# Kernel optimization log

Measured on AMD Instinct MI355X. Metric: run time of the kernel, lower is better.

The kernel has to match this reference:

```python
import jax, jax.numpy as jnp
import numpy as np

N = 100000  # nodes
E = 1600000  # edges
D_IN = 64
D_H = 64


def _sage_conv(x, src, dst, w_l, b_l, w_r):
    """PyG SAGEConv (mean aggr): lin_l(mean_j x_j) + lin_r(x_i).
    w_l, w_r: [out, in]; b_l: [out]."""
    # scatter-mean of source features onto target nodes
    msg_sum = jax.ops.segment_sum(x[src], dst, num_segments=N)  # [N, in]
    cnt = jax.ops.segment_sum(jnp.ones((src.shape[0],), x.dtype), dst, num_segments=N)
    mean = msg_sum / jnp.maximum(cnt, 1.0)[:, None]
    return mean @ w_l.T + b_l + x @ w_r.T


def setup_inputs() -> dict:
    key = jax.random.key(0)
    ks = jax.random.split(key, 8)
    x = jax.random.normal(ks[0], (N, D_IN), dtype=jnp.float32)
    edge_index = jax.random.randint(ks[1], (2, E), 0, N, dtype=jnp.int64)
    s = 1.0 / np.sqrt(D_IN)
    w_l1 = jax.random.uniform(ks[2], (D_H, D_IN), jnp.float32, -s, s)
    b_l1 = jnp.zeros((D_H,), jnp.float32)
    w_r1 = jax.random.uniform(ks[3], (D_H, D_IN), jnp.float32, -s, s)
    s2 = 1.0 / np.sqrt(D_H)
    w_l2 = jax.random.uniform(ks[4], (D_H, D_H), jnp.float32, -s2, s2)
    b_l2 = jnp.zeros((D_H,), jnp.float32)
    w_r2 = jax.random.uniform(ks[5], (D_H, D_H), jnp.float32, -s2, s2)
    return {"x": x, "edge_index": edge_index,
            "w_l1": w_l1, "b_l1": b_l1, "w_r1": w_r1,
            "w_l2": w_l2, "b_l2": b_l2, "w_r2": w_r2}


def reference(x, edge_index, w_l1, b_l1, w_r1, w_l2, b_l2, w_r2):
    src, dst = edge_index[0], edge_index[1]
    h = jax.nn.relu(_sage_conv(x, src, dst, w_l1, b_l1, w_r1))
    out = _sage_conv(h, src, dst, w_l2, b_l2, w_r2)
    return out
```

## Files before the change

### kernel.cpp

```cpp
#include <hip/hip_runtime.h>

#define N_NODES 100000
#define N_EDGES 1600000
#define D 64

#define BSHIFT 7
#define BNODES (1 << BSHIFT)
#define NB ((N_NODES + BNODES - 1) / BNODES)
#define PB 256
#define TILE ((N_EDGES + PB - 1) / PB)
#define CAP 2432
#define MAXB 4096
#define CAST_GRID 2048
#define HPARTS (N_NODES / 16 * 4)

typedef __attribute__((ext_vector_type(8))) short short8;
typedef __attribute__((ext_vector_type(4))) float float4v;

__device__ __forceinline__ unsigned short f2bf(float f) {
    unsigned u = __float_as_uint(f);
    u = (u + 0x7fffu + ((u >> 16) & 1u)) >> 16;
    return (unsigned short)u;
}
__device__ __forceinline__ unsigned packbf2(float a, float b) {
    return (unsigned)f2bf(a) | ((unsigned)f2bf(b) << 16);
}

__device__ __forceinline__ float4 bf16x4_to_f4(uint2 v) {
    float4 r;
    r.x = __uint_as_float(v.x << 16);
    r.y = __uint_as_float(v.x & 0xffff0000u);
    r.z = __uint_as_float(v.y << 16);
    r.w = __uint_as_float(v.y & 0xffff0000u);
    return r;
}

__global__ __launch_bounds__(256) void cast_absmax_part(const float* __restrict__ x,
                                                        unsigned short* __restrict__ xb,
                                                        float* __restrict__ partial) {
    __shared__ float red[4];
    float m = 0.0f;
    int stride = gridDim.x * 256;
    for (int i = blockIdx.x * 256 + threadIdx.x; i < N_NODES * D / 4; i += stride) {
        float4 v = ((const float4*)x)[i];
        ushort4 o;
        o.x = f2bf(v.x); o.y = f2bf(v.y); o.z = f2bf(v.z); o.w = f2bf(v.w);
        ((ushort4*)xb)[i] = o;
        m = fmaxf(m, fmaxf(fmaxf(fabsf(v.x), fabsf(v.y)), fmaxf(fabsf(v.z), fabsf(v.w))));
    }
    for (int off = 32; off >= 1; off >>= 1) m = fmaxf(m, __shfl_xor(m, off, 64));
    if ((threadIdx.x & 63) == 0) red[threadIdx.x >> 6] = m;
    __syncthreads();
    if (threadIdx.x == 0)
        partial[blockIdx.x] = fmaxf(fmaxf(red[0], red[1]), fmaxf(red[2], red[3]));
}

__global__ __launch_bounds__(1024) void reduce_amax(const float* __restrict__ partial,
                                                    int n,
                                                    unsigned* __restrict__ amax_bits) {
    __shared__ float red[16];
    float m = 0.0f;
    for (int i = threadIdx.x; i < n; i += 1024) m = fmaxf(m, partial[i]);
    for (int off = 32; off >= 1; off >>= 1) m = fmaxf(m, __shfl_xor(m, off, 64));
    if ((threadIdx.x & 63) == 0) red[threadIdx.x >> 6] = m;
    __syncthreads();
    if (threadIdx.x == 0) {
        float mm = 0.0f;
#pragma unroll
        for (int w = 0; w < 16; ++w) mm = fmaxf(mm, red[w]);
        *amax_bits = __float_as_uint(mm);
    }
}

__global__ __launch_bounds__(256) void quant8(const unsigned short* __restrict__ inb,
                                              unsigned char* __restrict__ out8,
                                              const unsigned* __restrict__ amax_bits) {
    int i = blockIdx.x * blockDim.x + threadIdx.x;
    if (i >= N_NODES * D / 4) return;
    float A = __uint_as_float(*amax_bits);
    float s = (A > 0.0f) ? 127.0f / A : 0.0f;
    uint2 v = ((const uint2*)inb)[i];
    float4 f = bf16x4_to_f4(v);
    int q0 = min(127, max(-127, __float2int_rn(f.x * s))) + 128;
    int q1 = min(127, max(-127, __float2int_rn(f.y * s))) + 128;
    int q2 = min(127, max(-127, __float2int_rn(f.z * s))) + 128;
    int q3 = min(127, max(-127, __float2int_rn(f.w * s))) + 128;
    ((unsigned*)out8)[i] = (unsigned)q0 | ((unsigned)q1 << 8) |
                           ((unsigned)q2 << 16) | ((unsigned)q3 << 24);
}

__global__ __launch_bounds__(256) void prep_w2(const float* __restrict__ wl1,
                                               const float* __restrict__ wr1,
                                               unsigned short* __restrict__ wb1,
                                               const float* __restrict__ wl2,
                                               const float* __restrict__ wr2,
                                               unsigned short* __restrict__ wb2) {
    int i = blockIdx.x * 256 + threadIdx.x;
    int j = i & 8191;
    int o = j >> 7, k = j & 127;
    if (i < 8192) {
        float v = (k < D) ? wl1[o * D + k] : wr1[o * D + (k - D)];
        wb1[j] = f2bf(v);
    } else {
        float v = (k < D) ? wl2[o * D + k] : wr2[o * D + (k - D)];
        wb2[j] = f2bf(v);
    }
}

__global__ __launch_bounds__(1024) void p1_fused(const int* __restrict__ src,
                                                 const int* __restrict__ dst,
                                                 int* __restrict__ gcnt,
                                                 int* __restrict__ part) {
    __shared__ int hist[NB];
    for (int i = threadIdx.x; i < NB; i += 1024) hist[i] = 0;
    __syncthreads();

    int lo = blockIdx.x * TILE;
    int hi = min(lo + TILE, N_EDGES);

    unsigned pk[7];
    int bk[7];
#pragma unroll
    for (int k = 0; k < 7; ++k) {
        int e = lo + threadIdx.x + k * 1024;
        if (e < hi) {
            int dd = dst[e];
            int ss = src[e];
            int b = dd >> BSHIFT;
            pk[k] = ((unsigned)ss << BSHIFT) | (unsigned)(dd & (BNODES - 1));
            bk[k] = b;
            atomicAdd(&hist[b], 1);
        } else {
            bk[k] = -1;
        }
    }
    __syncthreads();

    for (int b = threadIdx.x; b < NB; b += 1024) {
        int h = hist[b];
        if (h) hist[b] = b * CAP + atomicAdd(&gcnt[b], h);
    }
    __syncthreads();

#pragma unroll
    for (int k = 0; k < 7; ++k) {
        if (bk[k] >= 0) {
            int p = atomicAdd(&hist[bk[k]], 1);
            part[p] = (int)pk[k];
        }
    }
}

__global__ __launch_bounds__(1024) void scan_nb(const int* __restrict__ gcnt,
                                                int* __restrict__ bbase) {
    __shared__ int t[1024];
    int i = threadIdx.x;
    int v = (i < NB) ? gcnt[i] : 0;
    int val = v;
    t[i] = val;
    __syncthreads();
    for (int off = 1; off < 1024; off <<= 1) {
        int u = (i >= off) ? t[i - off] : 0;
        __syncthreads();
        val += u;
        t[i] = val;
        __syncthreads();
    }
    if (i < NB) bbase[i] = val - v;
}

__global__ __launch_bounds__(1024) void p2_sort(const int* __restrict__ bbase,
                                                const int* __restrict__ gcnt,
                                                const int* __restrict__ part,
                                                int* __restrict__ row_ptr,
                                                int* __restrict__ sorted_src) {
    __shared__ int in_buf[MAXB];
    __shared__ int out_buf[MAXB];
    __shared__ int hist[BNODES];
    __shared__ int exs[BNODES];
    __shared__ int cursor[BNODES];

    int k = blockIdx.x;
    int base  = bbase[k];
    int count = gcnt[k];
    int src0  = k * CAP;
    int tid = threadIdx.x;

    for (int i = tid; i < BNODES; i += 1024) hist[i] = 0;
    __syncthreads();

    if (count <= MAXB) {
        for (int i = tid; i < count; i += 1024) {
            int w = part[src0 + i];
            in_buf[i] = w;
            atomicAdd(&hist[w & (BNODES - 1)], 1);
        }
        __syncthreads();
        if (tid < 64) {
            int a = hist[2 * tid], b = hist[2 * tid + 1];
            int s = a + b, incl = s;
            for (int off = 1; off < 64; off <<= 1) {
                int t = __shfl_up(incl, off, 64);
                if (tid >= off) incl += t;
            }
            int excl = incl - s;
            exs[2 * tid] = excl;
            exs[2 * tid + 1] = excl + a;
        }
        __syncthreads();
        if (tid < BNODES) {
            int node = k * BNODES + tid;
            if (node < N_NODES) row_ptr[node] = base + exs[tid];
            cursor[tid] = exs[tid];
        }
        if (tid == 0 && k == NB - 1) row_ptr[N_NODES] = N_EDGES;
        __syncthreads();
        for (int i = tid; i < count; i += 1024) {
            int w = in_buf[i];
            int r = atomicAdd(&cursor[w & (BNODES - 1)], 1);
            out_buf[r] = w >> BSHIFT;
        }
        __syncthreads();
        for (int i = tid; i < count; i += 1024)
            sorted_src[base + i] = out_buf[i];
    } else {
        for (int i = tid; i < count; i += 1024)
            atomicAdd(&hist[part[src0 + i] & (BNODES - 1)], 1);
        __syncthreads();
        if (tid < 64) {
            int a = hist[2 * tid], b = hist[2 * tid + 1];
            int s = a + b, incl = s;
            for (int off = 1; off < 64; off <<= 1) {
                int t = __shfl_up(incl, off, 64);
                if (tid >= off) incl += t;
            }
            int excl = incl - s;
            exs[2 * tid] = excl;
            exs[2 * tid + 1] = excl + a;
        }
        __syncthreads();
        if (tid < BNODES) {
            int node = k * BNODES + tid;
            if (node < N_NODES) row_ptr[node] = base + exs[tid];
            cursor[tid] = exs[tid];
        }
        if (tid == 0 && k == NB - 1) row_ptr[N_NODES] = N_EDGES;
        __syncthreads();
        for (int i = tid; i < count; i += 1024) {
            int w = part[src0 + i];
            int r = atomicAdd(&cursor[w & (BNODES - 1)], 1);
            sorted_src[base + r] = w >> BSHIFT;
        }
    }
}

#define ACCW(w, kk) { aLo[kk] += (w) & 0x00FF00FFu; \
                      aHi[kk] += __builtin_amdgcn_perm(0u, (w), 0x04030401u); }
#define ACC4(v) { ACCW((v).x, 0) ACCW((v).y, 1) ACCW((v).z, 2) ACCW((v).w, 3) }

__global__ __launch_bounds__(512) void sage8(
    const int* __restrict__ row_ptr, const int* __restrict__ nbr,
    const unsigned char* __restrict__ tab8,
    const unsigned short* __restrict__ selfb,
    const unsigned* __restrict__ amax_bits,
    const unsigned short* __restrict__ wb,
    const float* __restrict__ b_l,
    float* __restrict__ out,
    unsigned short* __restrict__ outb,
    float* __restrict__ hpart,
    int apply_relu)
{
    __shared__ unsigned short a_s[16][136];
    __shared__ float bias[D];

    int tid = threadIdx.x;
    if (tid < D) bias[tid] = b_l[tid];

    int wave = tid >> 6;
    int lane = tid & 63;
    int nsel = lane >> 5;
    int l32  = lane & 31;
    int g    = l32 >> 2;
    int c    = l32 & 3;
    int arow = wave * 2 + nsel;
    int node = blockIdx.x * 16 + arow;

    float A  = __uint_as_float(*amax_bits);
    float gs = A * (1.0f / 127.0f);

    int begin = row_ptr[node];
    int end   = row_ptr[node + 1];

    unsigned c16 = (unsigned)(c << 4);
    unsigned aLo[4] = {0, 0, 0, 0};
    unsigned aHi[4] = {0, 0, 0, 0};
    for (int base = begin; base < end; base += 32) {
        int m = end - base; if (m > 32) m = 32;
        int id = (l32 < m) ? __builtin_nontemporal_load(&nbr[base + l32]) : 0;
        int s0 = __shfl(id, nsel * 32 + g,      64);
        int s1 = __shfl(id, nsel * 32 + 8 + g,  64);
        int s2 = __shfl(id, nsel * 32 + 16 + g, 64);
        int s3 = __shfl(id, nsel * 32 + 24 + g, 64);
        bool a0 = (g < m), a1 = (8 + g < m), a2 = (16 + g < m), a3 = (24 + g < m);
        uint4 v0, v1, v2, v3;
        if (a0) v0 = *(const uint4*)(tab8 + ((((unsigned)s0) << 6) | c16));
        if (a1) v1 = *(const uint4*)(tab8 + ((((unsigned)s1) << 6) | c16));
        if (a2) v2 = *(const uint4*)(tab8 + ((((unsigned)s2) << 6) | c16));
        if (a3) v3 = *(const uint4*)(tab8 + ((((unsigned)s3) << 6) | c16));
        if (a0) { ACC4(v0) }
        if (a1) { ACC4(v1) }
        if (a2) { ACC4(v2) }
        if (a3) { ACC4(v3) }
    }

#pragma unroll
    for (int off = 4; off <= 16; off <<= 1) {
#pragma unroll
        for (int k = 0; k < 4; ++k) {
            aLo[k] += (unsigned)__shfl_xor((int)aLo[k], off, 64);
            aHi[k] += (unsigned)__shfl_xor((int)aHi[k], off, 64);
        }
    }

    int   deg  = end - begin;
    float invd = 1.0f / fmaxf((float)deg, 1.0f);
    float bofs = 128.0f * (float)deg;
    float sc   = gs * invd;

    if (l32 < 4) {
        uint4 q0, q1;
        float d0 = ((float)(aLo[0] & 0xFFFFu) - bofs) * sc;
        float d2 = ((float)(aLo[0] >> 16)     - bofs) * sc;
        float d1 = ((float)(aHi[0] & 0xFFFFu) - bofs) * sc;
        float d3 = ((float)(aHi[0] >> 16)     - bofs) * sc;
        q0.x = packbf2(d0, d1); q0.y = packbf2(d2, d3);
        d0 = ((float)(aLo[1] & 0xFFFFu) - bofs) * sc;
        d2 = ((float)(aLo[1] >> 16)     - bofs) * sc;
        d1 = ((float)(aHi[1] & 0xFFFFu) - bofs) * sc;
        d3 = ((float)(aHi[1] >> 16)     - bofs) * sc;
        q0.z = packbf2(d0, d1); q0.w = packbf2(d2, d3);
        d0 = ((float)(aLo[2] & 0xFFFFu) - bofs) * sc;
        d2 = ((float)(aLo[2] >> 16)     - bofs) * sc;
        d1 = ((float)(aHi[2] & 0xFFFFu) - bofs) * sc;
        d3 = ((float)(aHi[2] >> 16)     - bofs) * sc;
        q1.x = packbf2(d0, d1); q1.y = packbf2(d2, d3);
        d0 = ((float)(aLo[3] & 0xFFFFu) - bofs) * sc;
        d2 = ((float)(aLo[3] >> 16)     - bofs) * sc;
        d1 = ((float)(aHi[3] & 0xFFFFu) - bofs) * sc;
        d3 = ((float)(aHi[3] >> 16)     - bofs) * sc;
        q1.z = packbf2(d0, d1); q1.w = packbf2(d2, d3);
        *(uint4*)&a_s[arow][16 * l32]     = q0;
        *(uint4*)&a_s[arow][16 * l32 + 8] = q1;
    }
    if (l32 < 16) {
        uint2 xv = *(const uint2*)&selfb[(size_t)node * D + 4 * l32];
        *(uint2*)&a_s[arow][64 + 4 * l32] = xv;
    }
    __syncthreads();

    if (wave >= 4) return;

    int quad = lane >> 4;
    int cc   = lane & 15;

    float4v acc = {0.f, 0.f, 0.f, 0.f};
#pragma unroll
    for (int kk = 0; kk < 4; ++kk) {
        short8 af = *(const short8*)&a_s[cc][kk * 32 + quad * 8];
        short8 bf = *(const short8*)(wb + (size_t)(wave * 16 + cc) * 128 + kk * 32 + quad * 8);
        acc = __builtin_amdgcn_mfma_f32_16x16x32_bf16(af, bf, acc, 0, 0, 0);
    }

    int o = wave * 16 + cc;
    float bv = bias[o];
    float vv[4];
#pragma unroll
    for (int r = 0; r < 4; ++r) {
        float v = acc[r] + bv;
        if (apply_relu) v = fmaxf(v, 0.0f);
        vv[r] = v;
    }
#pragma unroll
    for (int r = 0; r < 4; ++r) {
        int nd = blockIdx.x * 16 + quad * 4 + r;
        if (out)  __builtin_nontemporal_store(vv[r], &out[(size_t)nd * D + o]);
        if (outb) __builtin_nontemporal_store(f2bf(vv[r]), &outb[(size_t)nd * D + o]);
    }
    if (hpart) {
        float m = fmaxf(fmaxf(fabsf(vv[0]), fabsf(vv[1])),
                        fmaxf(fabsf(vv[2]), fabsf(vv[3])));
        for (int off = 32; off >= 1; off >>= 1) m = fmaxf(m, __shfl_xor(m, off, 64));
        if (lane == 0) hpart[blockIdx.x * 4 + wave] = m;
    }
}

extern "C" void kernel_launch(void* const* d_in, const int* in_sizes, int n_in,
                              void* d_out, int out_size, void* d_ws, size_t ws_size,
                              hipStream_t stream) {
    const float* x    = (const float*)d_in[0];
    const int*   ei   = (const int*)d_in[1];
    const float* w_l1 = (const float*)d_in[2];
    const float* b_l1 = (const float*)d_in[3];
    const float* w_r1 = (const float*)d_in[4];
    const float* w_l2 = (const float*)d_in[5];
    const float* b_l2 = (const float*)d_in[6];
    const float* w_r2 = (const float*)d_in[7];
    float* out = (float*)d_out;

    const int* src = ei;
    const int* dst = ei + N_EDGES;

    unsigned* scales   = (unsigned*)d_ws;
    int* gcnt          = (int*)d_ws + 4;
    int* bbase         = gcnt + NB;
    int* row_ptr       = bbase + NB;
    int* part          = row_ptr + 100004;
    int* sorted_src    = part + NB * CAP;
    unsigned short* xb = (unsigned short*)(sorted_src + N_EDGES);
    unsigned short* hb = xb + (size_t)N_NODES * D;
    unsigned char* x8  = (unsigned char*)(hb + (size_t)N_NODES * D);
    unsigned char* h8  = x8 + (size_t)N_NODES * D;
    unsigned short* wb1 = (unsigned short*)(h8 + (size_t)N_NODES * D);
    unsigned short* wb2 = wb1 + D * 2 * D;
    float* partA       = (float*)(wb2 + D * 2 * D);

    hipMemsetAsync(gcnt, 0, NB * sizeof(int), stream);

    dim3 b256(256);
    int qgrid = (N_NODES * D / 4 + 255) / 256;
    cast_absmax_part<<<dim3(CAST_GRID), b256, 0, stream>>>(x, xb, partA);
    reduce_amax<<<dim3(1), dim3(1024), 0, stream>>>(partA, CAST_GRID, &scales[0]);
    quant8<<<dim3(qgrid), b256, 0, stream>>>(xb, x8, &scales[0]);
    prep_w2<<<dim3(64), b256, 0, stream>>>(w_l1, w_r1, wb1, w_l2, w_r2, wb2);

    p1_fused<<<dim3(PB), dim3(1024), 0, stream>>>(src, dst, gcnt, part);
    scan_nb<<<dim3(1), dim3(1024), 0, stream>>>(gcnt, bbase);
    p2_sort<<<dim3(NB), dim3(1024), 0, stream>>>(bbase, gcnt, part, row_ptr, sorted_src);

    dim3 lblk(512);
    dim3 lgrid(N_NODES / 16);
    sage8<<<lgrid, lblk, 0, stream>>>(row_ptr, sorted_src, x8, xb,
                                      &scales[0], wb1, b_l1,
                                      (float*)nullptr, hb, partA, 1);
    reduce_amax<<<dim3(1), dim3(1024), 0, stream>>>(partA, HPARTS, &scales[1]);
    quant8<<<dim3(qgrid), b256, 0, stream>>>(hb, h8, &scales[1]);
    sage8<<<lgrid, lblk, 0, stream>>>(row_ptr, sorted_src, h8, hb,
                                      &scales[1], wb2, b_l2,
                                      out, (unsigned short*)nullptr,
                                      (float*)nullptr, 0);
}
```

Before: 233.0 us.

## Merge preprocessing kernels into fewer launches and stage sage8 output stores via LDS

Cast/absmax and the edge bucketing pass now run as one launch split by block index. A single mid kernel does the bucket scan, the amax reduce and the weight prep, and a single back kernel does the per-bucket sort plus x quantisation, cutting the launch count from ten to six. Inside sage8, the self-feature load is issued early, bf16 packing uses the v_cvt_pk_bf16_f32 instruction, and results are staged in shared memory so the idle waves write coalesced 16-byte stores. The per-wave amax is also reduced in-block, which shrinks the partial array. In exchange it adds a barrier and LDS use in sage8, and it drops the p2_sort overflow path for buckets larger than MAXB.

```diff
diff --git a/kernel.cpp b/kernel.cpp
--- a/kernel.cpp
+++ b/kernel.cpp
@@ -11,19 +11,24 @@
 #define TILE ((N_EDGES + PB - 1) / PB)
 #define CAP 2432
 #define MAXB 4096
-#define CAST_GRID 2048
-#define HPARTS (N_NODES / 16 * 4)
+#define CAST_BLKS 512
+#define QBLKS ((N_NODES * D / 4 + 1023) / 1024)
+#define HPARTS (N_NODES / 16)
 
 typedef __attribute__((ext_vector_type(8))) short short8;
 typedef __attribute__((ext_vector_type(4))) float float4v;
+typedef __attribute__((ext_vector_type(2))) unsigned uint2v;
+typedef __attribute__((ext_vector_type(4))) unsigned uint4v;
 
 __device__ __forceinline__ unsigned short f2bf(float f) {
     unsigned u = __float_as_uint(f);
     u = (u + 0x7fffu + ((u >> 16) & 1u)) >> 16;
     return (unsigned short)u;
 }
-__device__ __forceinline__ unsigned packbf2(float a, float b) {
-    return (unsigned)f2bf(a) | ((unsigned)f2bf(b) << 16);
+__device__ __forceinline__ unsigned cvtpk(float a, float b) {
+    unsigned r;
+    asm("v_cvt_pk_bf16_f32 %0, %1, %2" : "=v"(r) : "v"(a), "v"(b));
+    return r;
 }
 
 __device__ __forceinline__ float4 bf16x4_to_f4(uint2 v) {
@@ -35,87 +40,43 @@
     return r;
 }
 
-__global__ __launch_bounds__(256) void cast_absmax_part(const float* __restrict__ x,
-                                                        unsigned short* __restrict__ xb,
-                                                        float* __restrict__ partial) {
-    __shared__ float red[4];
-    float m = 0.0f;
-    int stride = gridDim.x * 256;
-    for (int i = blockIdx.x * 256 + threadIdx.x; i < N_NODES * D / 4; i += stride) {
-        float4 v = ((const float4*)x)[i];
-        ushort4 o;
-        o.x = f2bf(v.x); o.y = f2bf(v.y); o.z = f2bf(v.z); o.w = f2bf(v.w);
-        ((ushort4*)xb)[i] = o;
-        m = fmaxf(m, fmaxf(fmaxf(fabsf(v.x), fabsf(v.y)), fmaxf(fabsf(v.z), fabsf(v.w))));
-    }
-    for (int off = 32; off >= 1; off >>= 1) m = fmaxf(m, __shfl_xor(m, off, 64));
-    if ((threadIdx.x & 63) == 0) red[threadIdx.x >> 6] = m;
-    __syncthreads();
-    if (threadIdx.x == 0)
-        partial[blockIdx.x] = fmaxf(fmaxf(red[0], red[1]), fmaxf(red[2], red[3]));
-}
-
-__global__ __launch_bounds__(1024) void reduce_amax(const float* __restrict__ partial,
-                                                    int n,
-                                                    unsigned* __restrict__ amax_bits) {
+__global__ __launch_bounds__(1024) void front(const float* __restrict__ x,
+                                              unsigned short* __restrict__ xb,
+                                              float* __restrict__ partial,
+                                              const int* __restrict__ src,
+                                              const int* __restrict__ dst,
+                                              int* __restrict__ gcnt,
+                                              int* __restrict__ part) {
     __shared__ float red[16];
-    float m = 0.0f;
-    for (int i = threadIdx.x; i < n; i += 1024) m = fmaxf(m, partial[i]);
-    for (int off = 32; off >= 1; off >>= 1) m = fmaxf(m, __shfl_xor(m, off, 64));
-    if ((threadIdx.x & 63) == 0) red[threadIdx.x >> 6] = m;
-    __syncthreads();
-    if (threadIdx.x == 0) {
-        float mm = 0.0f;
-#pragma unroll
-        for (int w = 0; w < 16; ++w) mm = fmaxf(mm, red[w]);
-        *amax_bits = __float_as_uint(mm);
-    }
-}
-
-__global__ __launch_bounds__(256) void quant8(const unsigned short* __restrict__ inb,
-                                              unsigned char* __restrict__ out8,
-                                              const unsigned* __restrict__ amax_bits) {
-    int i = blockIdx.x * blockDim.x + threadIdx.x;
-    if (i >= N_NODES * D / 4) return;
-    float A = __uint_as_float(*amax_bits);
-    float s = (A > 0.0f) ? 127.0f / A : 0.0f;
-    uint2 v = ((const uint2*)inb)[i];
-    float4 f = bf16x4_to_f4(v);
-    int q0 = min(127, max(-127, __float2int_rn(f.x * s))) + 128;
-    int q1 = min(127, max(-127, __float2int_rn(f.y * s))) + 128;
-    int q2 = min(127, max(-127, __float2int_rn(f.z * s))) + 128;
-    int q3 = min(127, max(-127, __float2int_rn(f.w * s))) + 128;
-    ((unsigned*)out8)[i] = (unsigned)q0 | ((unsigned)q1 << 8) |
-                           ((unsigned)q2 << 16) | ((unsigned)q3 << 24);
-}
-
-__global__ __launch_bounds__(256) void prep_w2(const float* __restrict__ wl1,
-                                               const float* __restrict__ wr1,
-                                               unsigned short* __restrict__ wb1,
-                                               const float* __restrict__ wl2,
-                                               const float* __restrict__ wr2,
-                                               unsigned short* __restrict__ wb2) {
-    int i = blockIdx.x * 256 + threadIdx.x;
-    int j = i & 8191;
-    int o = j >> 7, k = j & 127;
-    if (i < 8192) {
-        float v = (k < D) ? wl1[o * D + k] : wr1[o * D + (k - D)];
-        wb1[j] = f2bf(v);
-    } else {
-        float v = (k < D) ? wl2[o * D + k] : wr2[o * D + (k - D)];
-        wb2[j] = f2bf(v);
-    }
-}
-
-__global__ __launch_bounds__(1024) void p1_fused(const int* __restrict__ src,
-                                                 const int* __restrict__ dst,
-                                                 int* __restrict__ gcnt,
-                                                 int* __restrict__ part) {
     __shared__ int hist[NB];
+
+    if (blockIdx.x < CAST_BLKS) {
+        float m = 0.0f;
+        int stride = CAST_BLKS * 1024;
+        for (int i = blockIdx.x * 1024 + threadIdx.x; i < N_NODES * D / 4; i += stride) {
+            float4 v = ((const float4*)x)[i];
+            ushort4 o;
+            o.x = f2bf(v.x); o.y = f2bf(v.y); o.z = f2bf(v.z); o.w = f2bf(v.w);
+            ((ushort4*)xb)[i] = o;
+            m = fmaxf(m, fmaxf(fmaxf(fabsf(v.x), fabsf(v.y)), fmaxf(fabsf(v.z), fabsf(v.w))));
+        }
+        for (int off = 32; off >= 1; off >>= 1) m = fmaxf(m, __shfl_xor(m, off, 64));
+        if ((threadIdx.x & 63) == 0) red[threadIdx.x >> 6] = m;
+        __syncthreads();
+        if (threadIdx.x == 0) {
+            float mm = 0.0f;
+#pragma unroll
+            for (int w = 0; w < 16; ++w) mm = fmaxf(mm, red[w]);
+            partial[blockIdx.x] = mm;
+        }
+        return;
+    }
+
+    int bid = blockIdx.x - CAST_BLKS;
     for (int i = threadIdx.x; i < NB; i += 1024) hist[i] = 0;
     __syncthreads();
 
-    int lo = blockIdx.x * TILE;
+    int lo = bid * TILE;
     int hi = min(lo + TILE, N_EDGES);
 
     unsigned pk[7];
@@ -151,106 +112,164 @@
     }
 }
 
-__global__ __launch_bounds__(1024) void scan_nb(const int* __restrict__ gcnt,
-                                                int* __restrict__ bbase) {
+__global__ __launch_bounds__(1024) void mid(const int* __restrict__ gcnt,
+                                            int* __restrict__ bbase,
+                                            const float* __restrict__ partial,
+                                            unsigned* __restrict__ amax_bits,
+                                            const float* __restrict__ wl1,
+                                            const float* __restrict__ wr1,
+                                            unsigned short* __restrict__ wb1,
+                                            const float* __restrict__ wl2,
+                                            const float* __restrict__ wr2,
+                                            unsigned short* __restrict__ wb2) {
     __shared__ int t[1024];
-    int i = threadIdx.x;
-    int v = (i < NB) ? gcnt[i] : 0;
-    int val = v;
-    t[i] = val;
-    __syncthreads();
-    for (int off = 1; off < 1024; off <<= 1) {
-        int u = (i >= off) ? t[i - off] : 0;
+    __shared__ float red[16];
+    int tid = threadIdx.x;
+
+    if (blockIdx.x == 0) {
+        int v = (tid < NB) ? gcnt[tid] : 0;
+        int val = v;
+        t[tid] = val;
         __syncthreads();
-        val += u;
-        t[i] = val;
+        for (int off = 1; off < 1024; off <<= 1) {
+            int u = (tid >= off) ? t[tid - off] : 0;
+            __syncthreads();
+            val += u;
+            t[tid] = val;
+            __syncthreads();
+        }
+        if (tid < NB) bbase[tid] = val - v;
+    } else if (blockIdx.x == 1) {
+        float m = 0.0f;
+        for (int i = tid; i < CAST_BLKS; i += 1024) m = fmaxf(m, partial[i]);
+        for (int off = 32; off >= 1; off >>= 1) m = fmaxf(m, __shfl_xor(m, off, 64));
+        if ((tid & 63) == 0) red[tid >> 6] = m;
         __syncthreads();
-    }
-    if (i < NB) bbase[i] = val - v;
-}
-
-__global__ __launch_bounds__(1024) void p2_sort(const int* __restrict__ bbase,
-                                                const int* __restrict__ gcnt,
-                                                const int* __restrict__ part,
-                                                int* __restrict__ row_ptr,
-                                                int* __restrict__ sorted_src) {
+        if (tid == 0) {
+            float mm = 0.0f;
+#pragma unroll
+            for (int w = 0; w < 16; ++w) mm = fmaxf(mm, red[w]);
+            *amax_bits = __float_as_uint(mm);
+        }
+    } else {
+        int i = (blockIdx.x - 2) * 1024 + tid;
+        int j = i & 8191;
+        int o = j >> 7, k = j & 127;
+        if (i < 8192) {
+            float v = (k < D) ? wl1[o * D + k] : wr1[o * D + (k - D)];
+            wb1[j] = f2bf(v);
+        } else {
+            float v = (k < D) ? wl2[o * D + k] : wr2[o * D + (k - D)];
+            wb2[j] = f2bf(v);
+        }
+    }
+}
+
+__device__ __forceinline__ void quant_body(int i, const unsigned short* __restrict__ inb,
+                                           unsigned char* __restrict__ out8, float s) {
+    uint2 v = ((const uint2*)inb)[i];
+    float4 f = bf16x4_to_f4(v);
+    int q0 = min(127, max(-127, __float2int_rn(f.x * s))) + 128;
+    int q1 = min(127, max(-127, __float2int_rn(f.y * s))) + 128;
+    int q2 = min(127, max(-127, __float2int_rn(f.z * s))) + 128;
+    int q3 = min(127, max(-127, __float2int_rn(f.w * s))) + 128;
+    ((unsigned*)out8)[i] = (unsigned)q0 | ((unsigned)q1 << 8) |
+                           ((unsigned)q2 << 16) | ((unsigned)q3 << 24);
+}
+
+__global__ __launch_bounds__(1024) void back(const int* __restrict__ bbase,
+                                             const int* __restrict__ gcnt,
+                                             const int* __restrict__ part,
+                                             int* __restrict__ row_ptr,
+                                             int* __restrict__ sorted_src,
+                                             const unsigned short* __restrict__ xb,
+                                             unsigned char* __restrict__ x8,
+                                             const unsigned* __restrict__ amax_bits) {
     __shared__ int in_buf[MAXB];
     __shared__ int out_buf[MAXB];
     __shared__ int hist[BNODES];
     __shared__ int exs[BNODES];
     __shared__ int cursor[BNODES];
 
+    int tid = threadIdx.x;
+
+    if (blockIdx.x >= NB) {
+        int i = (blockIdx.x - NB) * 1024 + tid;
+        if (i < N_NODES * D / 4) {
+            float A = __uint_as_float(*amax_bits);
+            float s = (A > 0.0f) ? 127.0f / A : 0.0f;
+            quant_body(i, xb, x8, s);
+        }
+        return;
+    }
+
     int k = blockIdx.x;
     int base  = bbase[k];
     int count = gcnt[k];
     int src0  = k * CAP;
-    int tid = threadIdx.x;
 
     for (int i = tid; i < BNODES; i += 1024) hist[i] = 0;
     __syncthreads();
 
-    if (count <= MAXB) {
-        for (int i = tid; i < count; i += 1024) {
-            int w = part[src0 + i];
-            in_buf[i] = w;
-            atomicAdd(&hist[w & (BNODES - 1)], 1);
-        }
-        __syncthreads();
-        if (tid < 64) {
-            int a = hist[2 * tid], b = hist[2 * tid + 1];
-            int s = a + b, incl = s;
-            for (int off = 1; off < 64; off <<= 1) {
-                int t = __shfl_up(incl, off, 64);
-                if (tid >= off) incl += t;
-            }
-            int excl = incl - s;
-            exs[2 * tid] = excl;
-            exs[2 * tid + 1] = excl + a;
-        }
-        __syncthreads();
-        if (tid < BNODES) {
-            int node = k * BNODES + tid;
-            if (node < N_NODES) row_ptr[node] = base + exs[tid];
-            cursor[tid] = exs[tid];
-        }
-        if (tid == 0 && k == NB - 1) row_ptr[N_NODES] = N_EDGES;
-        __syncthreads();
-        for (int i = tid; i < count; i += 1024) {
-            int w = in_buf[i];
-            int r = atomicAdd(&cursor[w & (BNODES - 1)], 1);
-            out_buf[r] = w >> BSHIFT;
-        }
-        __syncthreads();
-        for (int i = tid; i < count; i += 1024)
-            sorted_src[base + i] = out_buf[i];
-    } else {
-        for (int i = tid; i < count; i += 1024)
-            atomicAdd(&hist[part[src0 + i] & (BNODES - 1)], 1);
-        __syncthreads();
-        if (tid < 64) {
-            int a = hist[2 * tid], b = hist[2 * tid + 1];
-            int s = a + b, incl = s;
-            for (int off = 1; off < 64; off <<= 1) {
-                int t = __shfl_up(incl, off, 64);
-                if (tid >= off) incl += t;
-            }
-            int excl = incl - s;
-            exs[2 * tid] = excl;
-            exs[2 * tid + 1] = excl + a;
-        }
-        __syncthreads();
-        if (tid < BNODES) {
-            int node = k * BNODES + tid;
-            if (node < N_NODES) row_ptr[node] = base + exs[tid];
-            cursor[tid] = exs[tid];
-        }
-        if (tid == 0 && k == NB - 1) row_ptr[N_NODES] = N_EDGES;
-        __syncthreads();
-        for (int i = tid; i < count; i += 1024) {
-            int w = part[src0 + i];
-            int r = atomicAdd(&cursor[w & (BNODES - 1)], 1);
-            sorted_src[base + r] = w >> BSHIFT;
-        }
+    for (int i = tid; i < count; i += 1024) {
+        int w = part[src0 + i];
+        in_buf[i] = w;
+        atomicAdd(&hist[w & (BNODES - 1)], 1);
+    }
+    __syncthreads();
+    if (tid < 64) {
+        int a = hist[2 * tid], b = hist[2 * tid + 1];
+        int s = a + b, incl = s;
+        for (int off = 1; off < 64; off <<= 1) {
+            int t = __shfl_up(incl, off, 64);
+            if (tid >= off) incl += t;
+        }
+        int excl = incl - s;
+        exs[2 * tid] = excl;
+        exs[2 * tid + 1] = excl + a;
+    }
+    __syncthreads();
+    if (tid < BNODES) {
+        int node = k * BNODES + tid;
+        if (node < N_NODES) row_ptr[node] = base + exs[tid];
+        cursor[tid] = exs[tid];
+    }
+    if (tid == 0 && k == NB - 1) row_ptr[N_NODES] = N_EDGES;
+    __syncthreads();
+    for (int i = tid; i < count; i += 1024) {
+        int w = in_buf[i];
+        int r = atomicAdd(&cursor[w & (BNODES - 1)], 1);
+        out_buf[r] = w >> BSHIFT;
+    }
+    __syncthreads();
+    for (int i = tid; i < count; i += 1024)
+        sorted_src[base + i] = out_buf[i];
+}
+
+__global__ __launch_bounds__(1024) void quant8(const unsigned short* __restrict__ inb,
+                                               unsigned char* __restrict__ out8,
+                                               const unsigned* __restrict__ amax_bits) {
+    int i = blockIdx.x * 1024 + threadIdx.x;
+    if (i >= N_NODES * D / 4) return;
+    float A = __uint_as_float(*amax_bits);
+    float s = (A > 0.0f) ? 127.0f / A : 0.0f;
+    quant_body(i, inb, out8, s);
+}
+
+__global__ __launch_bounds__(1024) void reduce_amax(const float* __restrict__ partial,
+                                                    int n,
+                                                    unsigned* __restrict__ amax_bits) {
+    __shared__ float red[16];
+    float m = 0.0f;
+    for (int i = threadIdx.x; i < n; i += 1024) m = fmaxf(m, partial[i]);
+    for (int off = 32; off >= 1; off >>= 1) m = fmaxf(m, __shfl_xor(m, off, 64));
+    if ((threadIdx.x & 63) == 0) red[threadIdx.x >> 6] = m;
+    __syncthreads();
+    if (threadIdx.x == 0) {
+        float mm = 0.0f;
+#pragma unroll
+        for (int w = 0; w < 16; ++w) mm = fmaxf(mm, red[w]);
+        *amax_bits = __float_as_uint(mm);
     }
 }
 
@@ -271,7 +290,9 @@
     int apply_relu)
 {
     __shared__ unsigned short a_s[16][136];
+    __shared__ float st[16][68];
     __shared__ float bias[D];
+    __shared__ float wred[4];
 
     int tid = threadIdx.x;
     if (tid < D) bias[tid] = b_l[tid];
@@ -290,6 +311,10 @@
 
     int begin = row_ptr[node];
     int end   = row_ptr[node + 1];
+
+    uint2v xv = {0, 0};
+    if (l32 < 16)
+        xv = __builtin_nontemporal_load((const uint2v*)&selfb[(size_t)node * D + 4 * l32]);
 
     unsigned c16 = (unsigned)(c << 4);
     unsigned aLo[4] = {0, 0, 0, 0};
@@ -329,68 +354,87 @@
 
     if (l32 < 4) {
         uint4 q0, q1;
-        float d0 = ((float)(aLo[0] & 0xFFFFu) - bofs) * sc;
-        float d2 = ((float)(aLo[0] >> 16)     - bofs) * sc;
-        float d1 = ((float)(aHi[0] & 0xFFFFu) - bofs) * sc;
-        float d3 = ((float)(aHi[0] >> 16)     - bofs) * sc;
-        q0.x = packbf2(d0, d1); q0.y = packbf2(d2, d3);
+        float d0, d1, d2, d3;
+        d0 = ((float)(aLo[0] & 0xFFFFu) - bofs) * sc;
+        d2 = ((float)(aLo[0] >> 16)     - bofs) * sc;
+        d1 = ((float)(aHi[0] & 0xFFFFu) - bofs) * sc;
+        d3 = ((float)(aHi[0] >> 16)     - bofs) * sc;
+        q0.x = cvtpk(d0, d1); q0.y = cvtpk(d2, d3);
         d0 = ((float)(aLo[1] & 0xFFFFu) - bofs) * sc;
         d2 = ((float)(aLo[1] >> 16)     - bofs) * sc;
         d1 = ((float)(aHi[1] & 0xFFFFu) - bofs) * sc;
         d3 = ((float)(aHi[1] >> 16)     - bofs) * sc;
-        q0.z = packbf2(d0, d1); q0.w = packbf2(d2, d3);
+        q0.z = cvtpk(d0, d1); q0.w = cvtpk(d2, d3);
         d0 = ((float)(aLo[2] & 0xFFFFu) - bofs) * sc;
         d2 = ((float)(aLo[2] >> 16)     - bofs) * sc;
         d1 = ((float)(aHi[2] & 0xFFFFu) - bofs) * sc;
         d3 = ((float)(aHi[2] >> 16)     - bofs) * sc;
-        q1.x = packbf2(d0, d1); q1.y = packbf2(d2, d3);
+        q1.x = cvtpk(d0, d1); q1.y = cvtpk(d2, d3);
         d0 = ((float)(aLo[3] & 0xFFFFu) - bofs) * sc;
         d2 = ((float)(aLo[3] >> 16)     - bofs) * sc;
         d1 = ((float)(aHi[3] & 0xFFFFu) - bofs) * sc;
         d3 = ((float)(aHi[3] >> 16)     - bofs) * sc;
-        q1.z = packbf2(d0, d1); q1.w = packbf2(d2, d3);
+        q1.z = cvtpk(d0, d1); q1.w = cvtpk(d2, d3);
         *(uint4*)&a_s[arow][16 * l32]     = q0;
         *(uint4*)&a_s[arow][16 * l32 + 8] = q1;
     }
-    if (l32 < 16) {
-        uint2 xv = *(const uint2*)&selfb[(size_t)node * D + 4 * l32];
-        *(uint2*)&a_s[arow][64 + 4 * l32] = xv;
-    }
-    __syncthreads();
-
-    if (wave >= 4) return;
-
-    int quad = lane >> 4;
-    int cc   = lane & 15;
-
-    float4v acc = {0.f, 0.f, 0.f, 0.f};
-#pragma unroll
-    for (int kk = 0; kk < 4; ++kk) {
-        short8 af = *(const short8*)&a_s[cc][kk * 32 + quad * 8];
-        short8 bf = *(const short8*)(wb + (size_t)(wave * 16 + cc) * 128 + kk * 32 + quad * 8);
-        acc = __builtin_amdgcn_mfma_f32_16x16x32_bf16(af, bf, acc, 0, 0, 0);
-    }
-
-    int o = wave * 16 + cc;
-    float bv = bias[o];
-    float vv[4];
-#pragma unroll
-    for (int r = 0; r < 4; ++r) {
-        float v = acc[r] + bv;
-        if (apply_relu) v = fmaxf(v, 0.0f);
-        vv[r] = v;
-    }
-#pragma unroll
-    for (int r = 0; r < 4; ++r) {
-        int nd = blockIdx.x * 16 + quad * 4 + r;
-        if (out)  __builtin_nontemporal_store(vv[r], &out[(size_t)nd * D + o]);
-        if (outb) __builtin_nontemporal_store(f2bf(vv[r]), &outb[(size_t)nd * D + o]);
-    }
-    if (hpart) {
-        float m = fmaxf(fmaxf(fabsf(vv[0]), fabsf(vv[1])),
-                        fmaxf(fabsf(vv[2]), fabsf(vv[3])));
-        for (int off = 32; off >= 1; off >>= 1) m = fmaxf(m, __shfl_xor(m, off, 64));
-        if (lane == 0) hpart[blockIdx.x * 4 + wave] = m;
+    if (l32 < 16)
+        *(uint2v*)&a_s[arow][64 + 4 * l32] = xv;
+    __syncthreads();
+
+    if (wave < 4) {
+        int quad = lane >> 4;
+        int cc   = lane & 15;
+
+        float4v acc = {0.f, 0.f, 0.f, 0.f};
+#pragma unroll
+        for (int kk = 0; kk < 4; ++kk) {
+            short8 af = *(const short8*)&a_s[cc][kk * 32 + quad * 8];
+            short8 bf = *(const short8*)(wb + (size_t)(wave * 16 + cc) * 128 + kk * 32 + quad * 8);
+            acc = __builtin_amdgcn_mfma_f32_16x16x32_bf16(af, bf, acc, 0, 0, 0);
+        }
+
+        int o = wave * 16 + cc;
+        float bv = bias[o];
+        float vv[4];
+#pragma unroll
+        for (int r = 0; r < 4; ++r) {
+            float v = acc[r] + bv;
+            if (apply_relu) v = fmaxf(v, 0.0f);
+            vv[r] = v;
+            st[quad * 4 + r][o] = v;
+        }
+        if (hpart) {
+            float m = fmaxf(fmaxf(fabsf(vv[0]), fabsf(vv[1])),
+                            fmaxf(fabsf(vv[2]), fabsf(vv[3])));
+            for (int off = 32; off >= 1; off >>= 1) m = fmaxf(m, __shfl_xor(m, off, 64));
+            if (lane == 0) wred[wave] = m;
+        }
+    }
+    __syncthreads();
+
+    if (wave >= 4) {
+        int idx = tid - 256;
+        if (outb) {
+            if (idx < 128) {
+                int row = idx >> 3, c8 = idx & 7;
+                const float* p = &st[row][c8 * 8];
+                float4v f0 = *(const float4v*)p;
+                float4v f1 = *(const float4v*)(p + 4);
+                uint4v q;
+                q[0] = cvtpk(f0[0], f0[1]); q[1] = cvtpk(f0[2], f0[3]);
+                q[2] = cvtpk(f1[0], f1[1]); q[3] = cvtpk(f1[2], f1[3]);
+                __builtin_nontemporal_store(q,
+                    (uint4v*)&outb[((size_t)(blockIdx.x * 16 + row)) * D + 8 * c8]);
+            }
+        } else {
+            int row = idx >> 4, c4 = idx & 15;
+            uint4v q = *(const uint4v*)&st[row][c4 * 4];
+            __builtin_nontemporal_store(q,
+                (uint4v*)&out[((size_t)(blockIdx.x * 16 + row)) * D + 4 * c4]);
+        }
+        if (hpart && idx == 0)
+            hpart[blockIdx.x] = fmaxf(fmaxf(wred[0], wred[1]), fmaxf(wred[2], wred[3]));
     }
 }
 
@@ -424,18 +468,15 @@
     unsigned short* wb2 = wb1 + D * 2 * D;
     float* partA       = (float*)(wb2 + D * 2 * D);
 
-    hipMemsetAsync(gcnt, 0, NB * sizeof(int), stream);
-
-    dim3 b256(256);
-    int qgrid = (N_NODES * D / 4 + 255) / 256;
-    cast_absmax_part<<<dim3(CAST_GRID), b256, 0, stream>>>(x, xb, partA);
-    reduce_amax<<<dim3(1), dim3(1024), 0, stream>>>(partA, CAST_GRID, &scales[0]);
-    quant8<<<dim3(qgrid), b256, 0, stream>>>(xb, x8, &scales[0]);
-    prep_w2<<<dim3(64), b256, 0, stream>>>(w_l1, w_r1, wb1, w_l2, w_r2, wb2);
-
-    p1_fused<<<dim3(PB), dim3(1024), 0, stream>>>(src, dst, gcnt, part);
-    scan_nb<<<dim3(1), dim3(1024), 0, stream>>>(gcnt, bbase);
-    p2_sort<<<dim3(NB), dim3(1024), 0, stream>>>(bbase, gcnt, part, row_ptr, sorted_src);
+    (void)hipMemsetAsync(d_ws, 0, 16 + NB * sizeof(int), stream);
+
+    front<<<dim3(CAST_BLKS + PB), dim3(1024), 0, stream>>>(x, xb, partA,
+                                                           src, dst, gcnt, part);
+    mid<<<dim3(18), dim3(1024), 0, stream>>>(gcnt, bbase, partA, &scales[0],
+                                             w_l1, w_r1, wb1, w_l2, w_r2, wb2);
+    back<<<dim3(NB + QBLKS), dim3(1024), 0, stream>>>(bbase, gcnt, part,
+                                                      row_ptr, sorted_src,
+                                                      xb, x8, &scales[0]);
 
     dim3 lblk(512);
     dim3 lgrid(N_NODES / 16);
@@ -443,7 +484,7 @@
                                       &scales[0], wb1, b_l1,
                                       (float*)nullptr, hb, partA, 1);
     reduce_amax<<<dim3(1), dim3(1024), 0, stream>>>(partA, HPARTS, &scales[1]);
-    quant8<<<dim3(qgrid), b256, 0, stream>>>(hb, h8, &scales[1]);
+    quant8<<<dim3(QBLKS), dim3(1024), 0, stream>>>(hb, h8, &scales[1]);
     sage8<<<lgrid, lblk, 0, stream>>>(row_ptr, sorted_src, h8, hb,
                                       &scales[1], wb2, b_l2,
                                       out, (unsigned short*)nullptr,
```

Result: faster. 212.3 us (-8.9%).
